# Kernel optimization log

Hardware: AMD Instinct MI355X
Metric: run time of the kernel (lower is better)

## Reference

```python
import jax, jax.numpy as jnp
import numpy as np
from jax import lax

TAU = 0.05
N_ITERS = 4
TOPL = 64


def l2norm(x, axis):
    return x / (jnp.linalg.norm(x, axis=axis, keepdims=True) + 1e-6)


def setup_inputs() -> dict:
    key = jax.random.key(0)
    ks = jax.random.split(key, 8)
    B, N, Ck, Cv, H, W, L = 2, 4, 64, 512, 64, 64, 256
    qk = jax.random.normal(ks[0], (B, Ck, H, W), jnp.float32)
    qv = jax.random.normal(ks[1], (B, Cv, H, W), jnp.float32)
    qv_mem = jax.random.normal(ks[2], (B, N, Cv, H, W), jnp.float32)
    masks = jax.random.uniform(ks[3], (B, N, 2, H, W), jnp.float32)
    # random_init: normal(0, sqrt(2/L)) then l2norm over Ck (dim=-2)
    kappa0 = jax.random.normal(ks[4], (B, N, 2, Ck, L), jnp.float32) * np.sqrt(2.0 / L).astype(np.float32)
    kappa0 = l2norm(kappa0, axis=-2)
    nu0 = jnp.zeros((B, N, 2, Cv, L), jnp.float32)
    zita0 = jnp.full((B, N, 2, 1, L), 1e-6, jnp.float32)
    Cin = 2 * Cv + 2 * TOPL  # 1152
    Wf = jax.random.normal(ks[5], (Cv, Cin, 3, 3), jnp.float32) * 0.02
    bf = jnp.zeros((Cv,), jnp.float32)
    Wa = jax.random.normal(ks[6], (Cv, Cin, 3, 3), jnp.float32) * 0.02
    ba = jnp.zeros((Cv,), jnp.float32)
    return {"qk": qk, "qv": qv, "qv_mem": qv_mem, "masks": masks,
            "kappa0": kappa0, "nu0": nu0, "zita0": zita0,
            "Wf": Wf, "bf": bf, "Wa": Wa, "ba": ba}


def reference(qk, qv, qv_mem, masks, kappa0, nu0, zita0, Wf, bf, Wa, ba):
    B, Ck, H, W = qk.shape
    N = masks.shape[1]
    Cv = qv.shape[1]
    L = kappa0.shape[-1]
    HW = H * W

    # ---- swem: EM iterations (torch runs these under no_grad) ----
    x = qk.reshape(B, 1, 1, Ck, HW)            # (B,1,1,Ck,HW)
    m = masks.reshape(B, N, 2, HW, 1)          # (B,N,2,HW,1)
    x_t = jnp.swapaxes(x, -2, -1)              # (B,1,1,HW,Ck)
    x_t_n = l2norm(x_t, axis=-1)

    weights = m
    kappa = kappa0
    z = None
    zita = None
    for i in range(N_ITERS):
        # swe_step: softmax((z - max)/tau) == softmax(z/tau), stable
        kn = l2norm(kappa, axis=-2)
        zz = jnp.matmul(x_t, kn)               # (B,N,2,HW,L)
        zz = jax.nn.softmax(zz / TAU, axis=-1) * weights
        # swm_step
        zita = zita0 + zz.sum(axis=-2, keepdims=True)            # (B,N,2,1,L)
        kappa = (zita0 * kappa0 + jnp.matmul(x, zz)) / zita      # (B,N,2,Ck,L)
        z = zz
        if i < N_ITERS - 1:
            # sww_step
            kn = l2norm(kappa, axis=-2)
            s = jnp.matmul(x_t_n, kn)                            # (B,N,2,HW,L)
            mx = jnp.max(s, axis=-1, keepdims=True)
            mx = jnp.max(mx, axis=2, keepdims=True)
            s_exp = jnp.exp((s - mx) / TAU)
            sum_exp = s_exp.sum(axis=-1, keepdims=True)          # (B,N,2,HW,1)
            props = sum_exp / sum_exp.sum(axis=2, keepdims=True)
            weights = m * (1.0 - props)

    mv_flat = qv_mem.reshape(B, N, 1, Cv, HW)                    # (B,N,1,Cv,HW)
    nu = (zita0 * nu0 + jnp.matmul(mv_flat, z)) / zita           # (B,N,2,Cv,L)

    # ---- matching / get_affinity ----
    qk_n = l2norm(qk, axis=1)
    mk = l2norm(kappa, axis=-2)
    qk_ = qk_n.reshape(B, 1, 1, Ck, HW)
    aff = jnp.matmul(jnp.swapaxes(mk, -2, -1), qk_)              # (B,N,2,L,HW)
    mx = jnp.max(aff, axis=2, keepdims=True)
    mx = jnp.max(mx, axis=3, keepdims=True)
    exp_aff = jnp.exp((aff - mx) / TAU)
    p_aff = exp_aff / exp_aff.sum(axis=(2, 3), keepdims=True)
    p_aff = p_aff.reshape(B, N, 2 * L, HW)

    # ---- perm_inv_feat: top-l over L, cumulative sums (vectorized) ----
    ea = exp_aff.reshape(B * N, 2, L, H, W)
    sorted_aff = lax.top_k(jnp.moveaxis(ea, 2, -1), TOPL)[0]     # (BN,2,H,W,TOPL) desc
    feat = jnp.cumsum(sorted_aff, axis=-1)
    Sf = feat[:, 0] / (feat[:, 0] + feat[:, 1])                  # (BN,H,W,TOPL)
    Sf = jnp.moveaxis(Sf, -1, 1)                                 # (BN,TOPL,H,W)
    S = jnp.concatenate([Sf, 1.0 - Sf], axis=1)                  # (BN,2*TOPL,H,W)

    # ---- memory readout ----
    mv2 = jnp.swapaxes(nu, 2, 3).reshape(B, N, Cv, 2 * L)
    mem_out = jnp.matmul(mv2, p_aff).reshape(B * N, Cv, H, W)

    qv_e = jnp.broadcast_to(qv[:, None], (B, N, Cv, H, W)).reshape(B * N, Cv, H, W)
    fin = jnp.concatenate([mem_out, qv_e, S], axis=1)            # (BN, 2*Cv+2*TOPL, H, W)

    # ---- FeatureFusionLayer: gated 3x3 convs ----
    dn = ('NCHW', 'OIHW', 'NCHW')
    f = lax.conv_general_dilated(fin, Wf, (1, 1), 'SAME', dimension_numbers=dn) + bf[None, :, None, None]
    a = lax.conv_general_dilated(fin, Wa, (1, 1), 'SAME', dimension_numbers=dn) + ba[None, :, None, None]
    return f * jax.nn.sigmoid(a)
```

## Files before the change

kernel.cpp:

```cpp
#include <hip/hip_runtime.h>
#include <hip/hip_bf16.h>
#include <math.h>


typedef __attribute__((ext_vector_type(8))) short bf16x8;
typedef __attribute__((ext_vector_type(4))) float f32x4;
typedef __attribute__((ext_vector_type(16))) float f32x16;

static __device__ __forceinline__ short f2b(float f){
  __hip_bfloat16 h = __float2bfloat16(f);
  short s; __builtin_memcpy(&s, &h, 2); return s;
}
static __device__ __forceinline__ unsigned pack2(float lo, float hi){
  return (unsigned)(unsigned short)f2b(lo) | ((unsigned)(unsigned short)f2b(hi) << 16);
}

static __device__ __forceinline__ float wred_max(float v){
  #pragma unroll
  for (int off = 32; off > 0; off >>= 1) v = fmaxf(v, __shfl_xor(v, off));
  return v;
}
static __device__ __forceinline__ float wred_sum(float v){
  #pragma unroll
  for (int off = 32; off > 0; off >>= 1) v += __shfl_xor(v, off);
  return v;
}

static __device__ __forceinline__ void gload_lds16(const short* g, short* l){
  __builtin_amdgcn_global_load_lds((const __attribute__((address_space(1))) unsigned int*)(g),
                                   (__attribute__((address_space(3))) unsigned int*)(l),
                                   16, 0, 0);
}

#define FMA16(X0,X1,X2,X3,KV) \
  acc[0]+=X0.x*KV; acc[1]+=X0.y*KV; acc[2]+=X0.z*KV; acc[3]+=X0.w*KV; \
  acc[4]+=X1.x*KV; acc[5]+=X1.y*KV; acc[6]+=X1.z*KV; acc[7]+=X1.w*KV; \
  acc[8]+=X2.x*KV; acc[9]+=X2.y*KV; acc[10]+=X2.z*KV; acc[11]+=X2.w*KV; \
  acc[12]+=X3.x*KV; acc[13]+=X3.y*KV; acc[14]+=X3.z*KV; acc[15]+=X3.w*KV;


__global__ void k_prep_x(const float* __restrict__ qk, float* __restrict__ xT, float* __restrict__ xTn){
  int idx = blockIdx.x*256 + threadIdx.x;
  int b = idx >> 12, hw = idx & 4095;
  float v[64]; float ss = 0.f;
  #pragma unroll
  for (int k=0;k<64;k++){ v[k] = qk[((size_t)b*64 + k)*4096 + hw]; ss += v[k]*v[k]; }
  float inv = 1.f/(sqrtf(ss) + 1e-6f);
  #pragma unroll
  for (int k=0;k<64;k++){ xT[(size_t)idx*64 + k] = v[k]; xTn[(size_t)idx*64 + k] = v[k]*inv; }
}

__global__ void k_init_w_kn(const float* __restrict__ masks, const float* __restrict__ kappa0,
                            float* __restrict__ wts, float* __restrict__ kn){
  int t = blockIdx.x*256 + threadIdx.x;
  if (t < 16*4096) wts[t] = masks[t];
  if (t < 16*256){
    int bng = t >> 8, l = t & 255;
    float ss = 0.f;
    #pragma unroll 4
    for (int k=0;k<64;k++){ float v = kappa0[((size_t)bng*64 + k)*256 + l]; ss += v*v; }
    float inv = 1.f/(sqrtf(ss) + 1e-6f);
    #pragma unroll 4
    for (int k=0;k<64;k++) kn[((size_t)bng*64 + k)*256 + l] = kappa0[((size_t)bng*64 + k)*256 + l]*inv;
  }
}

__global__ __launch_bounds__(256) void k_prep_wt2b(const float* __restrict__ Wf, const float* __restrict__ Wa,
                                                   short* __restrict__ Wt2){
  __shared__ float wsl[64][145];
  int blk = blockIdx.x;
  int conv = blk & 1;
  int tile = blk >> 1;
  int cb = tile % 72;
  int cvb = tile / 72;
  const float* Wsrc = conv ? Wa : Wf;
  int t = threadIdx.x;
  int cvl = t >> 2, part = t & 3;
  const float* src = Wsrc + ((size_t)(cvb*64 + cvl)*1152 + cb*16)*9;
  #pragma unroll
  for (int i = 0; i < 9; i++){
    float4 v = *(const float4*)(src + part*4 + i*16);
    wsl[cvl][part*4 + i*16 + 0] = v.x;
    wsl[cvl][part*4 + i*16 + 1] = v.y;
    wsl[cvl][part*4 + i*16 + 2] = v.z;
    wsl[cvl][part*4 + i*16 + 3] = v.w;
  }
  __syncthreads();
  short* obase = Wt2 + ((size_t)tile*2 + conv)*9216;
  #pragma unroll
  for (int i = 0; i < 5; i++){
    int item = t + i*256;
    if (item < 1152){
      int rk = item >> 6;
      int r = rk >> 1, kh = rk & 1;
      int c2 = item & 63;
      bf16x8 v;
      #pragma unroll
      for (int j = 0; j < 8; j++)
        v[j] = f2b(wsl[c2][(kh*8 + j)*9 + r]);
      *(bf16x8*)(obase + (size_t)item*8) = v;
    }
  }
}

__global__ void k_qv_fin(const float* __restrict__ qv, unsigned* __restrict__ fin32){
  int t = blockIdx.x*256 + threadIdx.x;
  int bn = t >> 20;
  int rem = t & 1048575;
  int p = rem >> 12;
  int hw = rem & 4095;
  int b = bn >> 2;
  float lo = qv[((size_t)b*512 + 2*p)*4096 + hw];
  float hi = qv[((size_t)b*512 + 2*p + 1)*4096 + hw];
  fin32[(size_t)bn*2359296 + (size_t)(256 + p)*4096 + hw] = pack2(lo, hi);
}


__global__ __launch_bounds__(256) void k_zz(const float* __restrict__ xT, const float* __restrict__ kn,
                                            const float* __restrict__ wts, float* __restrict__ zzb){
  int blk = blockIdx.x;
  int bng = blk >> 8;
  int hw0 = (blk & 255) * 16;
  int b = bng >> 3;
  int t = threadIdx.x;
  int lane = t & 63, wid = t >> 6;
  __shared__ float xs[64][16];
  __shared__ float redm[4], reds[4];
  {
    int k = t & 63, pq = t >> 6;
    #pragma unroll
    for (int p = pq; p < 16; p += 4)
      xs[k][p] = xT[((size_t)b*4096 + hw0 + p)*64 + k];
  }
  float acc[16];
  #pragma unroll
  for (int p=0;p<16;p++) acc[p] = 0.f;
  __syncthreads();
  const float* knp = kn + (size_t)bng*16384 + t;
  #pragma unroll 2
  for (int k=0;k<64;k++){
    float knv = knp[k*256];
    float4 x0 = *(const float4*)&xs[k][0];
    float4 x1 = *(const float4*)&xs[k][4];
    float4 x2 = *(const float4*)&xs[k][8];
    float4 x3 = *(const float4*)&xs[k][12];
    FMA16(x0,x1,x2,x3,knv)
  }
  #pragma unroll
  for (int p=0;p<16;p++){
    float v = acc[p];
    float m = wred_max(v);
    if (lane==0) redm[wid] = m;
    __syncthreads();
    m = fmaxf(fmaxf(redm[0],redm[1]), fmaxf(redm[2],redm[3]));
    float e = __expf((v - m) * 20.0f);
    float s = wred_sum(e);
    if (lane==0) reds[wid] = s;
    __syncthreads();
    s = reds[0]+reds[1]+reds[2]+reds[3];
    float wgt = wts[bng*4096 + hw0 + p];
    zzb[((size_t)bng*4096 + hw0 + p)*256 + t] = e/s*wgt;
  }
}

__global__ __launch_bounds__(1024) void k_part(const float* __restrict__ qk, const float* __restrict__ zzb,
                                               float* __restrict__ kpart, float* __restrict__ zpart){
  int bng = blockIdx.x >> 4, ch = blockIdx.x & 15;
  int b = bng >> 3;
  int t = threadIdx.x; int l = t & 255; int kq = t >> 8;
  __shared__ float xs[64][80];
  __shared__ float zlds[16][256];
  float acc[16];
  #pragma unroll
  for (int j=0;j<16;j++) acc[j]=0.f;
  float zs = 0.f;
  for (int sc=0; sc<4; sc++){
    int hwb = ch*256 + sc*64;
    __syncthreads();
    {
      int hw_l = t & 63, kk = t >> 6;
      #pragma unroll
      for (int k = kk; k < 64; k += 16)
        xs[hw_l][k] = qk[((size_t)b*64 + k)*4096 + hwb + hw_l];
    }
    for (int chunk=0; chunk<4; chunk++){
      #pragma unroll
      for (int i=0;i<4;i++){
        int e = t + i*1024;
        int hh = e >> 8, l2 = e & 255;
        zlds[hh][l2] = zzb[((size_t)bng*4096 + hwb + chunk*16 + hh)*256 + l2];
      }
      __syncthreads();
      #pragma unroll 2
      for (int hh=0; hh<16; hh++){
        int hw_l = chunk*16 + hh;
        float zv = zlds[hh][l];
        zs += zv;
        const float* xp = &xs[hw_l][kq*16];
        float4 x0 = *(const float4*)(xp);
        float4 x1 = *(const float4*)(xp+4);
        float4 x2 = *(const float4*)(xp+8);
        float4 x3 = *(const float4*)(xp+12);
        FMA16(x0,x1,x2,x3,zv)
      }
      __syncthreads();
    }
  }
  #pragma unroll
  for (int j=0;j<16;j++)
    kpart[(((size_t)bng*16 + ch)*64 + kq*16 + j)*256 + l] = acc[j];
  if (kq == 0) zpart[((size_t)bng*16 + ch)*256 + l] = zs;
}

__global__ __launch_bounds__(1024) void k_fin(const float* __restrict__ kpart, const float* __restrict__ zpart,
                                              const float* __restrict__ kappa0, const float* __restrict__ zita0,
                                              float* __restrict__ kn, float* __restrict__ zita){
  int bng = blockIdx.x; int t = threadIdx.x; int l = t & 255; int kq = t >> 8;
  float z0 = zita0[bng*256 + l];
  float zs = z0;
  #pragma unroll
  for (int ch=0; ch<16; ch++) zs += zpart[((size_t)bng*16 + ch)*256 + l];
  if (kq==0) zita[bng*256 + l] = zs;
  float inv = 1.f/zs;
  float kap[16]; float ss = 0.f;
  #pragma unroll
  for (int j=0;j<16;j++){
    int k = kq*16 + j;
    float a = z0 * kappa0[((size_t)bng*64 + k)*256 + l];
    #pragma unroll
    for (int ch=0; ch<16; ch++) a += kpart[(((size_t)bng*16 + ch)*64 + k)*256 + l];
    float kv = a*inv; kap[j] = kv; ss += kv*kv;
  }
  __shared__ float ssr[4][256];
  ssr[kq][l] = ss;
  __syncthreads();
  float tot = ssr[0][l]+ssr[1][l]+ssr[2][l]+ssr[3][l];
  float ninv = 1.f/(sqrtf(tot) + 1e-6f);
  #pragma unroll
  for (int j=0;j<16;j++) kn[((size_t)bng*64 + kq*16 + j)*256 + l] = kap[j]*ninv;
}

__global__ __launch_bounds__(512) void k_sww(const float* __restrict__ xTn, const float* __restrict__ kn,
                                             const float* __restrict__ masks, float* __restrict__ wts){
  int blk = blockIdx.x;
  int bnI = blk >> 8;
  int hw0 = (blk & 255)*16;
  int b = bnI >> 2;
  int t = threadIdx.x;
  int lane = t & 63, wid = t >> 6;
  int g = t >> 8; int l = t & 255;
  int bng = bnI*2 + g;
  __shared__ float xs[64][16];
  __shared__ float redm[8], reds[8];
  {
    int k = t & 63, pq = t >> 6;
    #pragma unroll
    for (int p = pq; p < 16; p += 8)
      xs[k][p] = xTn[((size_t)b*4096 + hw0 + p)*64 + k];
  }
  float knr[64];
  const float* knp = kn + (size_t)bng*16384 + l;
  #pragma unroll
  for (int k=0;k<64;k++) knr[k] = knp[k*256];
  float acc[16];
  #pragma unroll
  for (int p=0;p<16;p++) acc[p]=0.f;
  __syncthreads();
  #pragma unroll 2
  for (int k=0;k<64;k++){
    float knv = knr[k];
    float4 x0 = *(const float4*)&xs[k][0];
    float4 x1 = *(const float4*)&xs[k][4];
    float4 x2 = *(const float4*)&xs[k][8];
    float4 x3 = *(const float4*)&xs[k][12];
    FMA16(x0,x1,x2,x3,knv)
  }
  #pragma unroll
  for (int p=0;p<16;p++){
    float v = acc[p];
    float m = wred_max(v);
    if (lane==0) redm[wid] = m;
    __syncthreads();
    m = fmaxf(fmaxf(fmaxf(redm[0],redm[1]),fmaxf(redm[2],redm[3])),
              fmaxf(fmaxf(redm[4],redm[5]),fmaxf(redm[6],redm[7])));
    float e = __expf((v - m) * 20.0f);
    float s = wred_sum(e);
    if (lane==0) reds[wid] = s;
    __syncthreads();
    float s0 = reds[0]+reds[1]+reds[2]+reds[3];
    float s1 = reds[4]+reds[5]+reds[6]+reds[7];
    if (lane==0 && (wid==0 || wid==4)){
      float sg = g ? s1 : s0;
      wts[bng*4096 + hw0 + p] = masks[bng*4096 + hw0 + p]*(1.f - sg/(s0+s1));
    }
  }
}

__global__ __launch_bounds__(512) void k_aff(const float* __restrict__ xTn, const float* __restrict__ kn,
                                             float* __restrict__ paff){
  int blk = blockIdx.x;
  int bnI = blk >> 8;
  int hw0 = (blk & 255)*16;
  int b = bnI >> 2;
  int t = threadIdx.x;
  int lane = t & 63, wid = t >> 6;
  int g = t >> 8; int l = t & 255;
  int bng = bnI*2 + g;
  __shared__ float xs[64][16];
  __shared__ float redm[8], reds[8];
  {
    int k = t & 63, pq = t >> 6;
    #pragma unroll
    for (int p = pq; p < 16; p += 8)
      xs[k][p] = xTn[((size_t)b*4096 + hw0 + p)*64 + k];
  }
  float knr[64];
  const float* knp = kn + (size_t)bng*16384 + l;
  #pragma unroll
  for (int k=0;k<64;k++) knr[k] = knp[k*256];
  float acc[16];
  #pragma unroll
  for (int p=0;p<16;p++) acc[p]=0.f;
  __syncthreads();
  #pragma unroll 2
  for (int k=0;k<64;k++){
    float knv = knr[k];
    float4 x0 = *(const float4*)&xs[k][0];
    float4 x1 = *(const float4*)&xs[k][4];
    float4 x2 = *(const float4*)&xs[k][8];
    float4 x3 = *(const float4*)&xs[k][12];
    FMA16(x0,x1,x2,x3,knv)
  }
  #pragma unroll
  for (int p=0;p<16;p++){
    float v = acc[p];
    float m = wred_max(v);
    if (lane==0) redm[wid] = m;
    __syncthreads();
    m = fmaxf(fmaxf(fmaxf(redm[0],redm[1]),fmaxf(redm[2],redm[3])),
              fmaxf(fmaxf(redm[4],redm[5]),fmaxf(redm[6],redm[7])));
    float e = __expf((v - m) * 20.0f);
    float s = wred_sum(e);
    if (lane==0) reds[wid] = s;
    __syncthreads();
    float tot = reds[0]+reds[1]+reds[2]+reds[3]+reds[4]+reds[5]+reds[6]+reds[7];
    paff[((size_t)bnI*4096 + hw0 + p)*512 + t] = e/tot;
  }
}


static __device__ __forceinline__ float topk_cum(float va, float vb, float vc, float vd, int lane){
  float run = 0.f, cme = 0.f;
  #pragma unroll 2
  for (int tt=0; tt<64; tt++){
    float m = fmaxf(fmaxf(va,vb), fmaxf(vc,vd));
    float wm = wred_max(m);
    run += wm;
    if (lane == tt) cme = run;
    unsigned long long ball = __ballot(m == wm);
    int wl = __ffsll(ball) - 1;
    if (lane == wl){
      if (va == wm) va = -1.f;
      else if (vb == wm) vb = -1.f;
      else if (vc == wm) vc = -1.f;
      else vd = -1.f;
    }
  }
  return cme;
}

__global__ __launch_bounds__(256) void k_topk(const float* __restrict__ paff, unsigned* __restrict__ fin32){
  int wid = threadIdx.x >> 6, lane = threadIdx.x & 63;
  int px = blockIdx.x*4 + wid;
  int bn = px >> 12, hw = px & 4095;
  const float* row = paff + (size_t)px*512;
  float4 a0 = *(const float4*)(row + lane*4);
  float4 a1 = *(const float4*)(row + 256 + lane*4);
  float c0 = topk_cum(a0.x,a0.y,a0.z,a0.w, lane);
  float c1 = topk_cum(a1.x,a1.y,a1.z,a1.w, lane);
  float sf = c0/(c0+c1);
  float sf2 = __shfl_down(sf, 1);
  if (!(lane & 1)){
    size_t base = (size_t)bn*2359296;
    fin32[base + (size_t)(512 + (lane>>1))*4096 + hw] = pack2(sf, sf2);
    fin32[base + (size_t)(544 + (lane>>1))*4096 + hw] = pack2(1.f - sf, 1.f - sf2);
  }
}


__global__ __launch_bounds__(256) void k_nu(const float* __restrict__ qvm, const float* __restrict__ zzb,
                                            const float* __restrict__ nu0, const float* __restrict__ zita0,
                                            const float* __restrict__ zita, short* __restrict__ mv2){
  constexpr int AP = 40;
  __shared__ short lA[64*AP];
  __shared__ short lB[128*AP];
  int blk = blockIdx.x;
  int bng = blk >> 4, cvb = (blk >> 1) & 7, lb = blk & 1;
  int bn = bng >> 1, g = bng & 1;
  int t = threadIdx.x, lane = t & 63, w = t >> 6;
  int wm = w >> 1, wn = w & 1;
  int quad = lane >> 4, fr = lane & 15;
  f32x4 acc[2][4] = {};
  const float* Ab = qvm + ((size_t)bn*512 + cvb*64)*4096;
  const float* Bb = zzb + (size_t)bng*4096*256 + lb*128;
  int arow = t >> 2, acg = (t & 3)*8;
  int bhw = t & 31, blg = (t >> 5)*8;
  for (int k0 = 0; k0 < 4096; k0 += 32){
    __syncthreads();
    {
      const float* s = Ab + (size_t)arow*4096 + k0 + acg;
      float4 f0 = *(const float4*)s, f1 = *(const float4*)(s+4);
      bf16x8 v;
      v[0]=f2b(f0.x); v[1]=f2b(f0.y); v[2]=f2b(f0.z); v[3]=f2b(f0.w);
      v[4]=f2b(f1.x); v[5]=f2b(f1.y); v[6]=f2b(f1.z); v[7]=f2b(f1.w);
      *(bf16x8*)&lA[arow*AP + acg] = v;
    }
    #pragma unroll
    for (int h = 0; h < 2; h++){
      int l0 = h*64 + blg;
      const float* s = Bb + (size_t)(k0 + bhw)*256 + l0;
      float4 f0 = *(const float4*)s, f1 = *(const float4*)(s+4);
      lB[(l0+0)*AP + bhw] = f2b(f0.x);
      lB[(l0+1)*AP + bhw] = f2b(f0.y);
      lB[(l0+2)*AP + bhw] = f2b(f0.z);
      lB[(l0+3)*AP + bhw] = f2b(f0.w);
      lB[(l0+4)*AP + bhw] = f2b(f1.x);
      lB[(l0+5)*AP + bhw] = f2b(f1.y);
      lB[(l0+6)*AP + bhw] = f2b(f1.z);
      lB[(l0+7)*AP + bhw] = f2b(f1.w);
    }
    __syncthreads();
    int koff = quad*8;
    bf16x8 a0 = *(const bf16x8*)&lA[(wm*32 +  0 + fr)*AP + koff];
    bf16x8 a1 = *(const bf16x8*)&lA[(wm*32 + 16 + fr)*AP + koff];
    #pragma unroll
    for (int nf=0; nf<4; nf++){
      bf16x8 bv = *(const bf16x8*)&lB[(wn*64 + nf*16 + fr)*AP + koff];
      acc[0][nf] = __builtin_amdgcn_mfma_f32_16x16x32_bf16(a0,bv,acc[0][nf],0,0,0);
      acc[1][nf] = __builtin_amdgcn_mfma_f32_16x16x32_bf16(a1,bv,acc[1][nf],0,0,0);
    }
  }
  #pragma unroll
  for (int mf=0; mf<2; mf++)
  #pragma unroll
  for (int nf=0; nf<4; nf++)
  #pragma unroll
  for (int r=0;r<4;r++){
    int cv = cvb*64 + wm*32 + mf*16 + quad*4 + r;
    int l  = lb*128 + wn*64 + nf*16 + fr;
    float c = acc[mf][nf][r];
    float z0 = zita0[bng*256 + l];
    float nv = (z0 * nu0[((size_t)bng*512 + cv)*256 + l] + c) / zita[bng*256 + l];
    mv2[((size_t)bn*512 + cv)*512 + g*256 + l] = f2b(nv);
  }
}

__global__ __launch_bounds__(256) void k_mem(const short* __restrict__ mv2, const float* __restrict__ paff,
                                             unsigned* __restrict__ fin32){
  constexpr int BP = 40;
  __shared__ short lB[256*BP];
  int blk = blockIdx.x;
  int bn = blk >> 7, cvb = (blk >> 4) & 7, hwb = blk & 15;
  int t = threadIdx.x, lane = t & 63, w = t >> 6;
  int quad = lane >> 4, fr = lane & 15;
  f32x4 acc[4][4] = {};
  const short* Ab = mv2 + ((size_t)bn*512 + cvb*64)*512;
  const float* Bb = paff + ((size_t)bn*4096 + hwb*256)*512;
  for (int k0=0; k0<512; k0+=32){
    __syncthreads();
    {
      const float* s = Bb + (size_t)t*512 + k0;
      #pragma unroll
      for (int q=0;q<4;q++){
        float4 f0 = *(const float4*)(s + q*8);
        float4 f1 = *(const float4*)(s + q*8 + 4);
        bf16x8 v;
        v[0]=f2b(f0.x); v[1]=f2b(f0.y); v[2]=f2b(f0.z); v[3]=f2b(f0.w);
        v[4]=f2b(f1.x); v[5]=f2b(f1.y); v[6]=f2b(f1.z); v[7]=f2b(f1.w);
        *(bf16x8*)&lB[t*BP + q*8] = v;
      }
    }
    __syncthreads();
    int koff = quad*8;
    bf16x8 af[4];
    #pragma unroll
    for (int mf=0; mf<4; mf++)
      af[mf] = *(const bf16x8*)(Ab + (size_t)(mf*16 + fr)*512 + k0 + koff);
    #pragma unroll
    for (int nf=0; nf<4; nf++){
      bf16x8 bv = *(const bf16x8*)&lB[(w*64 + nf*16 + fr)*BP + koff];
      #pragma unroll
      for (int mf=0; mf<4; mf++)
        acc[mf][nf] = __builtin_amdgcn_mfma_f32_16x16x32_bf16(af[mf], bv, acc[mf][nf],0,0,0);
    }
  }
  #pragma unroll
  for (int mf=0;mf<4;mf++)
  #pragma unroll
  for (int nf=0;nf<4;nf++){
    int hw = hwb*256 + w*64 + nf*16 + fr;
    int p0 = cvb*32 + mf*8 + quad*2;
    unsigned lo = pack2(acc[mf][nf][0], acc[mf][nf][1]);
    unsigned hi = pack2(acc[mf][nf][2], acc[mf][nf][3]);
    fin32[(size_t)bn*2359296 + (size_t)p0*4096 + hw] = lo;
    fin32[(size_t)bn*2359296 + (size_t)(p0+1)*4096 + hw] = hi;
  }
}


#define CONV_STAGE_DECL \
  unsigned stg[3][4];
#define CONV_LOAD_STG(CB) { \
    _Pragma("unroll") \
    for (int i = 0; i < 3; i++){ \
      int tk = wv*3 + i; \
      int skh = (tk >= 6) ? 1 : 0; \
      int srow = tk - skh*6; \
      int gy = y0 - 1 + srow; \
      bool ok = (gy >= 0 && gy < 64); \
      _Pragma("unroll") \
      for (int pj = 0; pj < 4; pj++) \
        stg[i][pj] = ok ? finB[(size_t)((CB)*8 + skh*4 + pj)*4096 + gy*64 + lane] : 0u; \
    } }
#define CONV_WRITE_STG { \
    _Pragma("unroll") \
    for (int i = 0; i < 3; i++){ \
      int tk = wv*3 + i; \
      int skh = (tk >= 6) ? 1 : 0; \
      int srow = tk - skh*6; \
      uint4 v; v.x = stg[i][0]; v.y = stg[i][1]; v.z = stg[i][2]; v.w = stg[i][3]; \
      *(uint4*)&lFu[((skh*6 + srow)*66 + lane + 1)*4] = v; \
    } }
#define CONV_DMA_W(CB) { \
    const short* src = Wslice + (size_t)(CB)*18432 + lane*8; \
    _Pragma("unroll") \
    for (int i = 0; i < 9; i++){ \
      int idx = wv*9 + i; \
      gload_lds16(src + idx*512, &wbuf[idx*512]); \
    } }
#define CONV_COMPUTE { \
    __builtin_amdgcn_s_setprio(1); \
    _Pragma("unroll 3") \
    for (int r9 = 0; r9 < 9; r9++){ \
      int dy = r9/3, dx = r9 - dy*3; \
      bf16x8 f0 = *(const bf16x8*)(wbuf + r9*1024 + kh*512 + ln*8); \
      bf16x8 f1 = *(const bf16x8*)(wbuf + r9*1024 + kh*512 + ln*8 + 256); \
      bf16x8 a0 = *(const bf16x8*)(wbuf + 9216 + r9*1024 + kh*512 + ln*8); \
      bf16x8 a1 = *(const bf16x8*)(wbuf + 9216 + r9*1024 + kh*512 + ln*8 + 256); \
      int row = wv + dy; \
      _Pragma("unroll") \
      for (int xh = 0; xh < 2; xh++){ \
        bf16x8 bv = *(const bf16x8*)((const short*)lFu + (((kh*6 + row)*66 + xh*32 + ln + dx)*8)); \
        accF[0][xh] = __builtin_amdgcn_mfma_f32_32x32x16_bf16(f0, bv, accF[0][xh],0,0,0); \
        accF[1][xh] = __builtin_amdgcn_mfma_f32_32x32x16_bf16(f1, bv, accF[1][xh],0,0,0); \
        accA[0][xh] = __builtin_amdgcn_mfma_f32_32x32x16_bf16(a0, bv, accA[0][xh],0,0,0); \
        accA[1][xh] = __builtin_amdgcn_mfma_f32_32x32x16_bf16(a1, bv, accA[1][xh],0,0,0); \
      } \
    } \
    __builtin_amdgcn_s_setprio(0); }
#define CONV_HALO_ZERO \
  if (t < 96){ \
    int pj = t & 3; int side = (t >> 2) & 1; int row = (t >> 3) % 6; int khz = t / 48; \
    lFu[((khz*6 + row)*66 + (side ? 65 : 0))*4 + pj] = 0u; \
  }

__global__ __launch_bounds__(256, 2) void k_convu(const unsigned* __restrict__ fin32,
                                                  const short* __restrict__ Wt2,
                                                  float* __restrict__ U){
  __shared__ __attribute__((aligned(16))) unsigned lFu[2*6*66*4];
  __shared__ __attribute__((aligned(16))) short wbuf[2*9216];
  int blk = blockIdx.x;
  int h = blk >> 8, b = (blk >> 7) & 1, cvb = (blk >> 4) & 7, yb = blk & 15;
  int t = threadIdx.x, lane = t & 63, wv = t >> 6;
  int ln = lane & 31, kh = lane >> 5;
  int y0 = yb*4;
  f32x16 accF[2][2] = {}, accA[2][2] = {};
  const unsigned* finB = fin32 + (size_t)(b*4)*2359296;
  const short* Wslice = Wt2 + (size_t)cvb*72*18432;
  CONV_HALO_ZERO
  CONV_STAGE_DECL
  for (int i = 0; i < 16; i++){
    int cb = 32 + h*16 + i;
    CONV_LOAD_STG(cb)
    __syncthreads();
    CONV_WRITE_STG
    CONV_DMA_W(cb)
    __syncthreads();
    CONV_COMPUTE
  }
  int y = y0 + wv;
  #pragma unroll
  for (int mf = 0; mf < 2; mf++)
  #pragma unroll
  for (int xh = 0; xh < 2; xh++){
    int x = xh*32 + ln;
    #pragma unroll
    for (int reg = 0; reg < 16; reg++){
      int cv = cvb*64 + mf*32 + 4*kh + 8*(reg>>2) + (reg&3);
      size_t o = (size_t)cv*4096 + (size_t)y*64 + x;
      U[((size_t)(h*2 + 0)*2 + b)*2097152 + o] = accF[mf][xh][reg];
      U[((size_t)(h*2 + 1)*2 + b)*2097152 + o] = accA[mf][xh][reg];
    }
  }
}

__global__ __launch_bounds__(256, 2) void k_conv(const unsigned* __restrict__ fin32,
                                                 const short* __restrict__ Wt2,
                                                 const float* __restrict__ bfv, const float* __restrict__ bav,
                                                 const float* __restrict__ U,
                                                 float* __restrict__ out){
  __shared__ __attribute__((aligned(16))) unsigned lFu[2*6*66*4];
  __shared__ __attribute__((aligned(16))) short wbuf[2*9216];
  int blk = blockIdx.x;
  int bn = blk >> 7, cvb = (blk >> 4) & 7, yb = blk & 15;
  int t = threadIdx.x, lane = t & 63, wv = t >> 6;
  int ln = lane & 31, kh = lane >> 5;
  int y0 = yb*4;
  f32x16 accF[2][2] = {}, accA[2][2] = {};
  const unsigned* finB = fin32 + (size_t)bn*2359296;
  const short* Wslice = Wt2 + (size_t)cvb*72*18432;
  CONV_HALO_ZERO
  CONV_STAGE_DECL
  for (int i = 0; i < 40; i++){
    int cb = (i < 32) ? i : i + 32;
    CONV_LOAD_STG(cb)
    __syncthreads();
    CONV_WRITE_STG
    CONV_DMA_W(cb)
    __syncthreads();
    CONV_COMPUTE
  }
  int y = y0 + wv;
  int b = bn >> 2;
  #pragma unroll
  for (int mf = 0; mf < 2; mf++)
  #pragma unroll
  for (int xh = 0; xh < 2; xh++){
    int x = xh*32 + ln;
    #pragma unroll
    for (int reg = 0; reg < 16; reg++){
      int cv = cvb*64 + mf*32 + 4*kh + 8*(reg>>2) + (reg&3);
      size_t o = (size_t)cv*4096 + (size_t)y*64 + x;
      float fv = accF[mf][xh][reg] + bfv[cv]
               + U[((size_t)0*2 + b)*2097152 + o] + U[((size_t)2*2 + b)*2097152 + o];
      float av = accA[mf][xh][reg] + bav[cv]
               + U[((size_t)1*2 + b)*2097152 + o] + U[((size_t)3*2 + b)*2097152 + o];
      out[((size_t)bn*512 + cv)*4096 + (size_t)y*64 + x] = fv/(1.f + __expf(-av));
    }
  }
}


extern "C" void kernel_launch(void* const* d_in, const int* in_sizes, int n_in,
                              void* d_out, int out_size, void* d_ws, size_t ws_size,
                              hipStream_t stream){
  const float* qk     = (const float*)d_in[0];
  const float* qv     = (const float*)d_in[1];
  const float* qvm    = (const float*)d_in[2];
  const float* masks  = (const float*)d_in[3];
  const float* kappa0 = (const float*)d_in[4];
  const float* nu0    = (const float*)d_in[5];
  const float* zita0  = (const float*)d_in[6];
  const float* Wf     = (const float*)d_in[7];
  const float* bfb    = (const float*)d_in[8];
  const float* Wa     = (const float*)d_in[9];
  const float* bab    = (const float*)d_in[10];
  float* out = (float*)d_out;

  float* ws    = (float*)d_ws;
  float* zzb   = ws;
  float* kpart = zzb + 16777216;
  float* zpart = kpart + 4194304;
  float* kn    = zpart + 65536;
  float* zita  = kn + 262144;
  float* wts   = zita + 4096;
  float* xT    = wts + 65536;
  float* xTn   = xT + 524288;
  short* mv2   = (short*)(xTn + 524288);
  unsigned* fin32 = (unsigned*)(mv2 + 4194304);
  short* Wt2   = (short*)(fin32 + 18874368);
  float* U     = zzb;

  k_prep_x<<<32, 256, 0, stream>>>(qk, xT, xTn);
  k_init_w_kn<<<256, 256, 0, stream>>>(masks, kappa0, wts, kn);
  k_prep_wt2b<<<1152, 256, 0, stream>>>(Wf, Wa, Wt2);
  k_qv_fin<<<32768, 256, 0, stream>>>(qv, fin32);

  for (int it = 0; it < 4; ++it){
    k_zz<<<4096, 256, 0, stream>>>(xT, kn, wts, zzb);
    k_part<<<256, 1024, 0, stream>>>(qk, zzb, kpart, zpart);
    k_fin<<<16, 1024, 0, stream>>>(kpart, zpart, kappa0, zita0, kn, zita);
    if (it < 3) k_sww<<<2048, 512, 0, stream>>>(xTn, kn, masks, wts);
  }

  k_nu<<<256, 256, 0, stream>>>(qvm, zzb, nu0, zita0, zita, mv2);
  k_aff<<<2048, 512, 0, stream>>>(xTn, kn, zzb );
  k_topk<<<8192, 256, 0, stream>>>(zzb, fin32);
  k_mem<<<1024, 256, 0, stream>>>(mv2, zzb, fin32);
  k_convu<<<512, 256, 0, stream>>>(fin32, Wt2, U);
  k_conv<<<1024, 256, 0, stream>>>(fin32, Wt2, bfb, bab, U, out);
}
```

Baseline: 2.223 ms.

## Fuse mask-weight update and next E-step into single swz kernel, widen k_fin grid

The separate k_sww weight update and the following k_zz E-step are merged into one k_swz kernel. It computes the normalized-x dot products once and derives both the softmax over the full 2L for the weights and the per-group softmax for zz. It rescales by the stored x norm to recover the unnormalized logits. k_fin is also spread over four times more blocks, each handling 64 L columns, so more CUs work on the reduction. The fused path depends on the unnormalized logits equalling norm times the normalized ones, which can differ slightly in rounding.

```diff
diff --git a/kernel.cpp b/kernel.cpp
--- a/kernel.cpp
+++ b/kernel.cpp
@@ -39,13 +39,16 @@
   acc[12]+=X3.x*KV; acc[13]+=X3.y*KV; acc[14]+=X3.z*KV; acc[15]+=X3.w*KV;
 
 
-__global__ void k_prep_x(const float* __restrict__ qk, float* __restrict__ xT, float* __restrict__ xTn){
+__global__ void k_prep_x(const float* __restrict__ qk, float* __restrict__ xT, float* __restrict__ xTn,
+                         float* __restrict__ xnrm){
   int idx = blockIdx.x*256 + threadIdx.x;
   int b = idx >> 12, hw = idx & 4095;
   float v[64]; float ss = 0.f;
   #pragma unroll
   for (int k=0;k<64;k++){ v[k] = qk[((size_t)b*64 + k)*4096 + hw]; ss += v[k]*v[k]; }
-  float inv = 1.f/(sqrtf(ss) + 1e-6f);
+  float nrm = sqrtf(ss) + 1e-6f;
+  float inv = 1.f/nrm;
+  xnrm[idx] = nrm;
   #pragma unroll
   for (int k=0;k<64;k++){ xT[(size_t)idx*64 + k] = v[k]; xTn[(size_t)idx*64 + k] = v[k]*inv; }
 }
@@ -160,6 +163,71 @@
     s = reds[0]+reds[1]+reds[2]+reds[3];
     float wgt = wts[bng*4096 + hw0 + p];
     zzb[((size_t)bng*4096 + hw0 + p)*256 + t] = e/s*wgt;
+  }
+}
+
+__global__ __launch_bounds__(512) void k_swz(const float* __restrict__ xTn, const float* __restrict__ kn,
+                                             const float* __restrict__ masks, const float* __restrict__ xnrm,
+                                             float* __restrict__ zzb){
+  int blk = blockIdx.x;
+  int bnI = blk >> 8;
+  int hw0 = (blk & 255)*16;
+  int b = bnI >> 2;
+  int t = threadIdx.x;
+  int lane = t & 63, wid = t >> 6;
+  int g = t >> 8; int l = t & 255;
+  int bng = bnI*2 + g;
+  __shared__ float xs[64][16];
+  __shared__ float xnr[16];
+  __shared__ float redm[8], reds[8], redz[8];
+  {
+    int k = t & 63, pq = t >> 6;
+    #pragma unroll
+    for (int p = pq; p < 16; p += 8)
+      xs[k][p] = xTn[((size_t)b*4096 + hw0 + p)*64 + k];
+  }
+  if (t < 16) xnr[t] = xnrm[b*4096 + hw0 + t];
+  float knr[64];
+  const float* knp = kn + (size_t)bng*16384 + l;
+  #pragma unroll
+  for (int k=0;k<64;k++) knr[k] = knp[k*256];
+  float acc[16];
+  #pragma unroll
+  for (int p=0;p<16;p++) acc[p]=0.f;
+  __syncthreads();
+  #pragma unroll 2
+  for (int k=0;k<64;k++){
+    float knv = knr[k];
+    float4 x0 = *(const float4*)&xs[k][0];
+    float4 x1 = *(const float4*)&xs[k][4];
+    float4 x2 = *(const float4*)&xs[k][8];
+    float4 x3 = *(const float4*)&xs[k][12];
+    FMA16(x0,x1,x2,x3,knv)
+  }
+  #pragma unroll
+  for (int p=0;p<16;p++){
+    float v = acc[p];
+    float m = wred_max(v);
+    if (lane==0) redm[wid] = m;
+    __syncthreads();
+    float mg0 = fmaxf(fmaxf(redm[0],redm[1]), fmaxf(redm[2],redm[3]));
+    float mg1 = fmaxf(fmaxf(redm[4],redm[5]), fmaxf(redm[6],redm[7]));
+    float mall = fmaxf(mg0, mg1);
+    float mg = g ? mg1 : mg0;
+    float nf = xnr[p];
+    float es = __expf((v - mall) * 20.0f);
+    float ez = __expf((v - mg) * 20.0f * nf);
+    float ssum = wred_sum(es);
+    float zsum = wred_sum(ez);
+    if (lane==0){ reds[wid] = ssum; redz[wid] = zsum; }
+    __syncthreads();
+    float s0 = reds[0]+reds[1]+reds[2]+reds[3];
+    float s1 = reds[4]+reds[5]+reds[6]+reds[7];
+    float szg = g ? (redz[4]+redz[5]+redz[6]+redz[7])
+                  : (redz[0]+redz[1]+redz[2]+redz[3]);
+    float sg = g ? s1 : s0;
+    float wgt = masks[bng*4096 + hw0 + p]*(1.f - sg/(s0+s1));
+    zzb[((size_t)bng*4096 + hw0 + p)*256 + l] = ez/szg*wgt;
   }
 }
 
@@ -215,85 +283,44 @@
 __global__ __launch_bounds__(1024) void k_fin(const float* __restrict__ kpart, const float* __restrict__ zpart,
                                               const float* __restrict__ kappa0, const float* __restrict__ zita0,
                                               float* __restrict__ kn, float* __restrict__ zita){
-  int bng = blockIdx.x; int t = threadIdx.x; int l = t & 255; int kq = t >> 8;
+  int bng = blockIdx.x >> 2, lq = blockIdx.x & 3;
+  int t = threadIdx.x;
+  int ll = t & 63, kq = t >> 6;
+  int l = lq*64 + ll;
+  __shared__ float invs[64];
+  __shared__ float ssr[16][64];
+  __shared__ float ninvs[64];
   float z0 = zita0[bng*256 + l];
-  float zs = z0;
-  #pragma unroll
-  for (int ch=0; ch<16; ch++) zs += zpart[((size_t)bng*16 + ch)*256 + l];
-  if (kq==0) zita[bng*256 + l] = zs;
-  float inv = 1.f/zs;
-  float kap[16]; float ss = 0.f;
-  #pragma unroll
-  for (int j=0;j<16;j++){
-    int k = kq*16 + j;
+  if (kq == 0){
+    float zs = z0;
+    #pragma unroll
+    for (int ch=0; ch<16; ch++) zs += zpart[((size_t)bng*16 + ch)*256 + l];
+    zita[bng*256 + l] = zs;
+    invs[ll] = 1.f/zs;
+  }
+  __syncthreads();
+  float inv = invs[ll];
+  float kap[4]; float ss = 0.f;
+  #pragma unroll
+  for (int j=0;j<4;j++){
+    int k = kq*4 + j;
     float a = z0 * kappa0[((size_t)bng*64 + k)*256 + l];
     #pragma unroll
     for (int ch=0; ch<16; ch++) a += kpart[(((size_t)bng*16 + ch)*64 + k)*256 + l];
     float kv = a*inv; kap[j] = kv; ss += kv*kv;
   }
-  __shared__ float ssr[4][256];
-  ssr[kq][l] = ss;
+  ssr[kq][ll] = ss;
   __syncthreads();
-  float tot = ssr[0][l]+ssr[1][l]+ssr[2][l]+ssr[3][l];
-  float ninv = 1.f/(sqrtf(tot) + 1e-6f);
-  #pragma unroll
-  for (int j=0;j<16;j++) kn[((size_t)bng*64 + kq*16 + j)*256 + l] = kap[j]*ninv;
-}
-
-__global__ __launch_bounds__(512) void k_sww(const float* __restrict__ xTn, const float* __restrict__ kn,
-                                             const float* __restrict__ masks, float* __restrict__ wts){
-  int blk = blockIdx.x;
-  int bnI = blk >> 8;
-  int hw0 = (blk & 255)*16;
-  int b = bnI >> 2;
-  int t = threadIdx.x;
-  int lane = t & 63, wid = t >> 6;
-  int g = t >> 8; int l = t & 255;
-  int bng = bnI*2 + g;
-  __shared__ float xs[64][16];
-  __shared__ float redm[8], reds[8];
-  {
-    int k = t & 63, pq = t >> 6;
-    #pragma unroll
-    for (int p = pq; p < 16; p += 8)
-      xs[k][p] = xTn[((size_t)b*4096 + hw0 + p)*64 + k];
-  }
-  float knr[64];
-  const float* knp = kn + (size_t)bng*16384 + l;
-  #pragma unroll
-  for (int k=0;k<64;k++) knr[k] = knp[k*256];
-  float acc[16];
-  #pragma unroll
-  for (int p=0;p<16;p++) acc[p]=0.f;
+  if (kq == 0){
+    float tot = 0.f;
+    #pragma unroll
+    for (int q=0;q<16;q++) tot += ssr[q][ll];
+    ninvs[ll] = 1.f/(sqrtf(tot) + 1e-6f);
+  }
   __syncthreads();
-  #pragma unroll 2
-  for (int k=0;k<64;k++){
-    float knv = knr[k];
-    float4 x0 = *(const float4*)&xs[k][0];
-    float4 x1 = *(const float4*)&xs[k][4];
-    float4 x2 = *(const float4*)&xs[k][8];
-    float4 x3 = *(const float4*)&xs[k][12];
-    FMA16(x0,x1,x2,x3,knv)
-  }
-  #pragma unroll
-  for (int p=0;p<16;p++){
-    float v = acc[p];
-    float m = wred_max(v);
-    if (lane==0) redm[wid] = m;
-    __syncthreads();
-    m = fmaxf(fmaxf(fmaxf(redm[0],redm[1]),fmaxf(redm[2],redm[3])),
-              fmaxf(fmaxf(redm[4],redm[5]),fmaxf(redm[6],redm[7])));
-    float e = __expf((v - m) * 20.0f);
-    float s = wred_sum(e);
-    if (lane==0) reds[wid] = s;
-    __syncthreads();
-    float s0 = reds[0]+reds[1]+reds[2]+reds[3];
-    float s1 = reds[4]+reds[5]+reds[6]+reds[7];
-    if (lane==0 && (wid==0 || wid==4)){
-      float sg = g ? s1 : s0;
-      wts[bng*4096 + hw0 + p] = masks[bng*4096 + hw0 + p]*(1.f - sg/(s0+s1));
-    }
-  }
+  float ninv = ninvs[ll];
+  #pragma unroll
+  for (int j=0;j<4;j++) kn[((size_t)bng*64 + kq*4 + j)*256 + l] = kap[j]*ninv;
 }
 
 __global__ __launch_bounds__(512) void k_aff(const float* __restrict__ xTn, const float* __restrict__ kn,
@@ -676,21 +703,22 @@
   float* wts   = zita + 4096;
   float* xT    = wts + 65536;
   float* xTn   = xT + 524288;
-  short* mv2   = (short*)(xTn + 524288);
+  float* xnrm  = xTn + 524288;
+  short* mv2   = (short*)(xnrm + 8192);
   unsigned* fin32 = (unsigned*)(mv2 + 4194304);
   short* Wt2   = (short*)(fin32 + 18874368);
   float* U     = zzb;
 
-  k_prep_x<<<32, 256, 0, stream>>>(qk, xT, xTn);
+  k_prep_x<<<32, 256, 0, stream>>>(qk, xT, xTn, xnrm);
   k_init_w_kn<<<256, 256, 0, stream>>>(masks, kappa0, wts, kn);
   k_prep_wt2b<<<1152, 256, 0, stream>>>(Wf, Wa, Wt2);
   k_qv_fin<<<32768, 256, 0, stream>>>(qv, fin32);
 
+  k_zz<<<4096, 256, 0, stream>>>(xT, kn, wts, zzb);
   for (int it = 0; it < 4; ++it){
-    k_zz<<<4096, 256, 0, stream>>>(xT, kn, wts, zzb);
     k_part<<<256, 1024, 0, stream>>>(qk, zzb, kpart, zpart);
-    k_fin<<<16, 1024, 0, stream>>>(kpart, zpart, kappa0, zita0, kn, zita);
-    if (it < 3) k_sww<<<2048, 512, 0, stream>>>(xTn, kn, masks, wts);
+    k_fin<<<64, 1024, 0, stream>>>(kpart, zpart, kappa0, zita0, kn, zita);
+    if (it < 3) k_swz<<<2048, 512, 0, stream>>>(xTn, kn, masks, xnrm, zzb);
   }
 
   k_nu<<<256, 256, 0, stream>>>(qvm, zzb, nu0, zita0, zita, mv2);
```

After: 1.959 ms. -11.9%, faster.
